# Kernel tuning notes

Measured on AMD Instinct MI355X. Metric: run time of the kernel, lower is better.

## Reference

```python
import jax, jax.numpy as jnp
import numpy as np

GROUP_SIZES = [5, 5, 5, 5, 5, 5, 4]  # 7 concept groups, sum = 34
LN_EPS = 1e-5


def setup_inputs() -> dict:
    key = jax.random.key(0)
    ks = jax.random.split(key, 12)
    B, N, D, K, P, C, NC, H = 256, 196, 768, 7, 512, 34, 7, 3072
    img_feat_map = jax.random.normal(ks[0], (B, N, D), dtype=jnp.float32)
    # torch: Embedding weight uniform in [-1/K, 1/K]
    vq_codebook = (jax.random.uniform(ks[1], (K, D), dtype=jnp.float32) * 2.0 - 1.0) / K
    agg_codebook = jax.random.normal(ks[2], (K, D), dtype=jnp.float32)
    W1 = jax.random.normal(ks[3], (D, H), dtype=jnp.float32) * 0.02
    b1 = jnp.zeros((H,), dtype=jnp.float32)
    W2 = jax.random.normal(ks[4], (H, D), dtype=jnp.float32) * 0.02
    b2 = jnp.zeros((D,), dtype=jnp.float32)
    ln_gamma = jnp.ones((D,), dtype=jnp.float32)
    ln_beta = jnp.zeros((D,), dtype=jnp.float32)
    W_proj = jax.random.normal(ks[5], (D, P), dtype=jnp.float32) * 0.02
    concept_emb = jax.random.normal(ks[6], (C, P), dtype=jnp.float32)
    concept_emb = concept_emb / jnp.linalg.norm(concept_emb, axis=-1, keepdims=True)
    cls_W = jax.random.normal(ks[7], (C, NC), dtype=jnp.float32) * 0.02
    cls_b = jnp.zeros((NC,), dtype=jnp.float32)
    logit_scale = jnp.float32(100.0)  # detached CLIP logit scale
    return {
        "img_feat_map": img_feat_map, "vq_codebook": vq_codebook,
        "agg_codebook": agg_codebook, "W1": W1, "b1": b1, "W2": W2, "b2": b2,
        "ln_gamma": ln_gamma, "ln_beta": ln_beta, "W_proj": W_proj,
        "concept_emb": concept_emb, "cls_W": cls_W, "cls_b": cls_b,
        "logit_scale": logit_scale,
    }


def _pairwise_sq_dists(x, cb):
    # x: [B, N, D], cb: [K, D] -> [B, N, K]
    x_sq = jnp.sum(x * x, axis=-1, keepdims=True)           # [B, N, 1]
    cb_sq = jnp.sum(cb * cb, axis=-1)                        # [K]
    dot = jnp.einsum("bnd,kd->bnk", x, cb)                  # [B, N, K]
    return x_sq + cb_sq - 2.0 * dot


def _avg_effective_rank(x, threshold=0.99):
    # x: [B, N, D]; per-sample SVD, rank = #{cumsum(S)/sum(S) <= thr}
    S = jnp.linalg.svd(jax.lax.stop_gradient(x), compute_uv=False)  # [B, min(N,D)]
    energy = jnp.cumsum(S, axis=-1) / jnp.sum(S, axis=-1, keepdims=True)
    ranks = jnp.sum(energy <= threshold, axis=-1)
    return jnp.mean(ranks.astype(jnp.float32))


def reference(img_feat_map, vq_codebook, agg_codebook, W1, b1, W2, b2,
              ln_gamma, ln_beta, W_proj, concept_emb, cls_W, cls_b, logit_scale):
    x = img_feat_map  # [B, N, D]

    avg_rank = _avg_effective_rank(x)

    # --- VectorQuantizeAggregator: soft assignment to 7 codes ---
    d_agg = _pairwise_sq_dists(x, agg_codebook)              # [B, N, K]
    soft = jax.nn.softmax(-d_agg, axis=-1)                   # [B, N, K]
    agg = jnp.einsum("bnk,bnd->bkd", soft, x)               # [B, K, D]

    # --- VectorQuantizer: hard argmin + gather (one-hot @ codebook) ---
    d_vq = _pairwise_sq_dists(x, vq_codebook)                # [B, N, K]
    idx = jnp.argmin(d_vq, axis=-1)                          # [B, N] int
    quantized = vq_codebook[idx]                             # [B, N, D] gather == onehot @ cb
    sg = jax.lax.stop_gradient
    codebook_loss = jnp.mean((quantized - sg(x)) ** 2)
    commitment_loss = jnp.mean((sg(quantized) - x) ** 2)
    vq_loss = codebook_loss + 1.0 * commitment_loss

    # --- bridge: FFN -> LayerNorm -> proj -> L2 normalize ---
    h = jax.nn.gelu(agg @ W1 + b1, approximate=False) @ W2 + b2  # [B, K, D]
    mu = jnp.mean(h, axis=-1, keepdims=True)
    var = jnp.mean((h - mu) ** 2, axis=-1, keepdims=True)
    hn = (h - mu) * jax.lax.rsqrt(var + LN_EPS) * ln_gamma + ln_beta
    tok = hn @ W_proj                                        # [B, K, 512]
    tok = tok / jnp.linalg.norm(tok, axis=-1, keepdims=True)

    # --- per-group concept logits: token g vs its concept slice ---
    logits_list = []
    start = 0
    for g, sz in enumerate(GROUP_SIZES):
        ce = concept_emb[start:start + sz]                   # [sz, 512]
        logits_list.append(logit_scale * (tok[:, g, :] @ ce.T))  # [B, sz]
        start += sz
    image_logits = jnp.concatenate(logits_list, axis=-1)     # [B, 34]

    cls_logits = image_logits @ cls_W + cls_b                # [B, 7]
    return (cls_logits, image_logits, vq_loss, avg_rank)
```

## Files before the change

kernel.cpp:

```cpp
#include <hip/hip_runtime.h>
#include <hip/hip_bf16.h>
#include <math.h>

using hbf = __hip_bfloat16;
typedef __bf16 bf16x8 __attribute__((ext_vector_type(8)));
typedef float f32x4 __attribute__((ext_vector_type(4)));

__device__ inline float wred(float v){
#pragma unroll
  for (int o = 32; o > 0; o >>= 1) v += __shfl_xor(v, o);
  return v;
}
__device__ inline float r16(float v){
  v += __shfl_xor(v, 1); v += __shfl_xor(v, 2);
  v += __shfl_xor(v, 4); v += __shfl_xor(v, 8);
  return v;
}
__device__ inline float fast_rcp(float x){
  float r; asm("v_rcp_f32 %0, %1" : "=v"(r) : "v"(x)); return r;
}
__device__ inline float d4(const float4& a, const float4& b){
  return a.x*b.x + a.y*b.y + a.z*b.z + a.w*b.w;
}

__global__ void k_init(float* scal){
  if (threadIdx.x < 2) scal[threadIdx.x] = 0.f;
}

__global__ __launch_bounds__(512) void k_dist(const float* __restrict__ x,
    const float* __restrict__ vqcb, const float* __restrict__ agcb,
    hbf* __restrict__ aggbf, float* __restrict__ scal){
  __shared__ float cA[5376];
  __shared__ float cV[5376];
  __shared__ float sqA[7], sqV[7];
  const int tid = threadIdx.x, lane = tid & 63, wave = tid >> 6;
  const int b = blockIdx.x;
  for (int i = tid; i < 5376; i += 512){ cA[i] = agcb[i]; cV[i] = vqcb[i]; }
  __syncthreads();
  {
    int grp = tid >> 4, l16 = tid & 15;
    if (grp < 14){
      const float* s = (grp < 7) ? &cA[grp*768] : &cV[(grp-7)*768];
      float acc = 0.f;
      for (int j = l16; j < 768; j += 16) acc += s[j]*s[j];
      acc = r16(acc);
      if (l16 == 0){ if (grp < 7) sqA[grp] = acc; else sqV[grp-7] = acc; }
    }
  }
  __syncthreads();
  float sqAr[7], sqVr[7];
#pragma unroll
  for (int k = 0; k < 7; ++k){ sqAr[k] = sqA[k]; sqVr[k] = sqV[k]; }

  float4 aR[7][3];
#pragma unroll
  for (int k = 0; k < 7; ++k)
#pragma unroll
    for (int c = 0; c < 3; ++c) aR[k][c] = make_float4(0.f,0.f,0.f,0.f);
  float loss = 0.f;

  const float* xb = x + (size_t)b*196*768;
  float4 cx0, cx1, cx2, nx0, nx1, nx2;
  { const float* p = xb + (size_t)wave*768 + (lane<<2);
    cx0 = *(const float4*)(p); cx1 = *(const float4*)(p+256); cx2 = *(const float4*)(p+512); }
  for (int it = 0; it < 25; ++it){
    const int n = it*8 + wave;
    const int nn = n + 8;
    if (nn < 196){
      const float* p = xb + (size_t)nn*768 + (lane<<2);
      nx0 = *(const float4*)(p); nx1 = *(const float4*)(p+256); nx2 = *(const float4*)(p+512);
    }
    if (n < 196){
      float xsq = d4(cx0,cx0)+d4(cx1,cx1)+d4(cx2,cx2);
      float dA[7], dV[7];
#pragma unroll
      for (int k = 0; k < 7; ++k){
        const float4* pa = (const float4*)&cA[k*768];
        const float4* pv = (const float4*)&cV[k*768];
        float4 a0 = pa[lane], a1 = pa[64+lane], a2 = pa[128+lane];
        float4 q0 = pv[lane], q1 = pv[64+lane], q2 = pv[128+lane];
        dA[k] = d4(cx0,a0)+d4(cx1,a1)+d4(cx2,a2);
        dV[k] = d4(cx0,q0)+d4(cx1,q1)+d4(cx2,q2);
      }
      xsq = wred(xsq);
#pragma unroll
      for (int k = 0; k < 7; ++k){ dA[k] = wred(dA[k]); dV[k] = wred(dV[k]); }
      float lg[7], mx = -1e30f;
#pragma unroll
      for (int k = 0; k < 7; ++k){ lg[k] = 2.f*dA[k] - sqAr[k]; mx = fmaxf(mx, lg[k]); }
      float pr[7], ssum = 0.f;
#pragma unroll
      for (int k = 0; k < 7; ++k){ pr[k] = expf(lg[k]-mx); ssum += pr[k]; }
      const float inv = 1.f/ssum;
      float mn = 1e30f;
#pragma unroll
      for (int k = 0; k < 7; ++k) mn = fminf(mn, sqVr[k] - 2.f*dV[k]);
      loss += xsq + mn;
#pragma unroll
      for (int k = 0; k < 7; ++k){
        const float w = pr[k]*inv;
        aR[k][0].x += w*cx0.x; aR[k][0].y += w*cx0.y; aR[k][0].z += w*cx0.z; aR[k][0].w += w*cx0.w;
        aR[k][1].x += w*cx1.x; aR[k][1].y += w*cx1.y; aR[k][1].z += w*cx1.z; aR[k][1].w += w*cx1.w;
        aR[k][2].x += w*cx2.x; aR[k][2].y += w*cx2.y; aR[k][2].z += w*cx2.z; aR[k][2].w += w*cx2.w;
      }
    }
    cx0 = nx0; cx1 = nx1; cx2 = nx2;
  }
  __syncthreads();
  for (int i = tid; i < 5376; i += 512) cA[i] = 0.f;
  __syncthreads();
  for (int w = 0; w < 8; ++w){
    if (wave == w){
#pragma unroll
      for (int k = 0; k < 7; ++k)
#pragma unroll
        for (int c = 0; c < 3; ++c){
          float* p = &cA[k*768 + c*256 + (lane<<2)];
          p[0] += aR[k][c].x; p[1] += aR[k][c].y; p[2] += aR[k][c].z; p[3] += aR[k][c].w;
        }
    }
    __syncthreads();
  }
  for (int i = tid; i < 5376; i += 512) aggbf[(size_t)b*5376 + i] = __float2bfloat16(cA[i]);
  if (lane == 0) atomicAdd(&scal[0], loss);
}

__global__ __launch_bounds__(512) void k_gram(const float* __restrict__ x, float* __restrict__ G){
  __shared__ hbf Xs[208*104];
  const int tid = threadIdx.x, lane = tid & 63, wave = tid >> 6;
  const int b = blockIdx.x;
  const int l15 = lane & 15;
  const int fr0 = wave, fr1 = wave + 8;
  const bool f1 = (fr1 < 13);
  f32x4 acc0[13] = {};
  f32x4 acc1[13] = {};
  const float* xb = x + (size_t)b*196*768;
  for (int kc = 0; kc < 8; ++kc){
    __syncthreads();
    for (int u = tid; u < 4992; u += 512){
      const int r = u / 24, c4 = u - r*24;
      ushort4 val;
      if (r < 196){
        float4 f = *(const float4*)(xb + (size_t)r*768 + kc*96 + c4*4);
        hbf t0 = __float2bfloat16(f.x), t1 = __float2bfloat16(f.y);
        hbf t2 = __float2bfloat16(f.z), t3 = __float2bfloat16(f.w);
        val.x = *(const unsigned short*)&t0; val.y = *(const unsigned short*)&t1;
        val.z = *(const unsigned short*)&t2; val.w = *(const unsigned short*)&t3;
      } else { val.x = 0; val.y = 0; val.z = 0; val.w = 0; }
      *(ushort4*)&Xs[r*104 + c4*4] = val;
    }
    __syncthreads();
#pragma unroll
    for (int kk = 0; kk < 3; ++kk){
      const int ko = kk*32 + (lane>>4)*8;
      bf16x8 a0 = *(const bf16x8*)&Xs[(fr0*16 + l15)*104 + ko];
      bf16x8 a1 = f1 ? *(const bf16x8*)&Xs[(fr1*16 + l15)*104 + ko] : a0;
#pragma unroll
      for (int fc = 0; fc < 13; ++fc){
        bf16x8 bb = *(const bf16x8*)&Xs[(fc*16 + l15)*104 + ko];
        acc0[fc] = __builtin_amdgcn_mfma_f32_16x16x32_bf16(a0, bb, acc0[fc], 0, 0, 0);
        if (f1) acc1[fc] = __builtin_amdgcn_mfma_f32_16x16x32_bf16(a1, bb, acc1[fc], 0, 0, 0);
      }
    }
  }
  const size_t gb = (size_t)b*38416;
  const int cr = (lane>>4)*4;
#pragma unroll
  for (int fc = 0; fc < 13; ++fc){
    const int gc = fc*16 + l15;
    if (gc < 196){
#pragma unroll
      for (int r = 0; r < 4; ++r){
        const int gr = fr0*16 + cr + r;
        if (gr < 196) G[gb + (size_t)gr*196 + gc] = acc0[fc][r];
      }
      if (f1){
#pragma unroll
        for (int r = 0; r < 4; ++r){
          const int gr = fr1*16 + cr + r;
          if (gr < 196) G[gb + (size_t)gr*196 + gc] = acc1[fc][r];
        }
      }
    }
  }
}

__global__ __launch_bounds__(1024) void k_eigen(const float* __restrict__ G, float* __restrict__ scal){
  extern __shared__ float S[];
  float* A   = S;
  float* ww  = S + 38496;
  float* dd  = S + 38752;
  float* ee  = S + 38952;
  float* e2  = S + 39152;
  float* red2= S + 39352;
  const int n = 196;
  const int tid = threadIdx.x, lane = tid & 63, wave = tid >> 6;
  const int grp = lane >> 4, c16 = lane & 15;
  const int b = blockIdx.x;
  {
    const float4* Gv = (const float4*)(G + (size_t)b*38416);
    float4* Av = (float4*)A;
    for (int u = tid; u < 9604; u += 1024) Av[u] = Gv[u];
    if (tid < 80) S[38416 + tid] = 0.f;
  }
  __syncthreads();
  for (int k = 0; k <= n-3; ++k){
    const int base = k + 1, m = n - 1 - k;
    const float* rowk = &A[(size_t)k*196];
    const float x0 = rowk[base];
    float4 v4[4];
    float sig = 0.f;
#pragma unroll
    for (int p = 0; p < 4; ++p){
      const int col = (p << 6) + (c16 << 2);
      float4 xv = *(const float4*)(rowk + col);
      xv.x = (col+0 > base && col+0 < n) ? xv.x : 0.f;
      xv.y = (col+1 > base && col+1 < n) ? xv.y : 0.f;
      xv.z = (col+2 > base && col+2 < n) ? xv.z : 0.f;
      xv.w = (col+3 > base && col+3 < n) ? xv.w : 0.f;
      v4[p] = xv;
      sig += xv.x*xv.x + xv.y*xv.y + xv.z*xv.z + xv.w*xv.w;
    }
    sig = r16(sig);
    float tau = 0.f, v0 = 0.f, alpha = x0;
    if (sig > 1e-20f){
      const float mu = sqrtf(x0*x0 + sig);
      alpha = (x0 > 0.f) ? -mu : mu;
      v0 = x0 - alpha;
      tau = 2.f/(sig + v0*v0);
    }
    if (tid == 0) ee[k] = alpha;
#pragma unroll
    for (int p = 0; p < 4; ++p){
      const int col = (p << 6) + (c16 << 2);
      v4[p].x = (col+0 == base) ? v0 : v4[p].x;
      v4[p].y = (col+1 == base) ? v0 : v4[p].y;
      v4[p].z = (col+2 == base) ? v0 : v4[p].z;
      v4[p].w = (col+3 == base) ? v0 : v4[p].w;
    }
    const int p0 = base >> 6;
    const int nsw = (m + 63) >> 6;
    if (tau != 0.f){
      float cpart = 0.f;
      for (int t = 0; t < nsw; ++t){
        const int i = (t << 6) + (wave << 2) + grp;
        float acc = 0.f;
        if (i < m){
          const float* Ar = &A[(size_t)(base+i)*196];
#pragma unroll
          for (int p = 0; p < 4; ++p){
            if (p >= p0){
              const int col = (p << 6) + (c16 << 2);
              const float4 a4 = *(const float4*)(Ar + col);
              acc += a4.x*v4[p].x + a4.y*v4[p].y + a4.z*v4[p].z + a4.w*v4[p].w;
            }
          }
        }
        acc = r16(acc);
        if (i < m && c16 == 0){
          const float wr = tau*acc;
          ww[base+i] = wr;
          cpart += ((i == 0) ? v0 : rowk[base+i])*wr;
        }
      }
      cpart += __shfl_xor(cpart, 16);
      cpart += __shfl_xor(cpart, 32);
      if (lane == 0) red2[wave] = cpart;
    }
    __syncthreads();
    if (tau != 0.f){
      const float4* r2 = (const float4*)red2;
      const float4 q0 = r2[0], q1 = r2[1], q2 = r2[2], q3 = r2[3];
      const float vtw = (q0.x+q0.y+q0.z+q0.w) + (q1.x+q1.y+q1.z+q1.w)
                      + (q2.x+q2.y+q2.z+q2.w) + (q3.x+q3.y+q3.z+q3.w);
      const float c2 = 0.5f*tau*vtw;
      float4 w4[4];
#pragma unroll
      for (int p = 0; p < 4; ++p){
        const int col = (p << 6) + (c16 << 2);
        const float4 t4 = *(const float4*)(ww + col);
        w4[p].x = (col+0 >= base && col+0 < n) ? (t4.x - c2*v4[p].x) : 0.f;
        w4[p].y = (col+1 >= base && col+1 < n) ? (t4.y - c2*v4[p].y) : 0.f;
        w4[p].z = (col+2 >= base && col+2 < n) ? (t4.z - c2*v4[p].z) : 0.f;
        w4[p].w = (col+3 >= base && col+3 < n) ? (t4.w - c2*v4[p].w) : 0.f;
      }
      for (int t = 0; t < nsw; ++t){
        const int i = (t << 6) + (wave << 2) + grp;
        if (i < m){
          const float vi = (i == 0) ? v0 : rowk[base+i];
          const float wi = ww[base+i] - c2*vi;
          float* Ar = &A[(size_t)(base+i)*196];
#pragma unroll
          for (int p = 0; p < 4; ++p){
            if (p >= p0){
              const int col = (p << 6) + (c16 << 2);
              float4 a4 = *(const float4*)(Ar + col);
              a4.x -= vi*w4[p].x + wi*v4[p].x;
              a4.y -= vi*w4[p].y + wi*v4[p].y;
              a4.z -= vi*w4[p].z + wi*v4[p].z;
              a4.w -= vi*w4[p].w + wi*v4[p].w;
              *(float4*)(Ar + col) = a4;
            }
          }
        }
      }
    }
    __syncthreads();
  }
  if (tid < n) dd[tid] = A[(size_t)tid*196 + tid];
  if (tid == 0) ee[n-2] = A[(size_t)(n-1)*196 + (n-2)];
  __syncthreads();
  if (tid < n-1) e2[tid] = ee[tid]*ee[tid];
  __syncthreads();
  float lo = 1e30f, hi = -1e30f;
  if (tid < n){
    const float rr = ((tid > 0) ? fabsf(ee[tid-1]) : 0.f) + ((tid < n-1) ? fabsf(ee[tid]) : 0.f);
    lo = dd[tid] - rr; hi = dd[tid] + rr;
  }
  {
    float l2 = lo, h2 = hi;
#pragma unroll
    for (int o = 32; o > 0; o >>= 1){
      l2 = fminf(l2, __shfl_xor(l2, o));
      h2 = fmaxf(h2, __shfl_xor(h2, o));
    }
    if (lane == 0){ ww[wave] = l2; red2[wave] = h2; }
  }
  __syncthreads();
  float glo = ww[0], ghi = red2[0];
#pragma unroll
  for (int w2 = 1; w2 < 16; ++w2){ glo = fminf(glo, ww[w2]); ghi = fmaxf(ghi, red2[w2]); }
  __syncthreads();
  float sv = 0.f;
  if (tid < n){
    float lob = glo, hib = ghi;
    for (int it2 = 0; it2 < 26; ++it2){
      const float mid = 0.5f*(lob + hib);
      float q = dd[0] - mid;
      int cnt = (q < 0.f) ? 1 : 0;
      for (int i = 1; i < n; ++i){
        const float r = fast_rcp(q);
        q = (dd[i] - mid) - e2[i-1]*r;
        q = (fabsf(q) < 1e-6f) ? -1e-6f : q;
        cnt += (q < 0.f) ? 1 : 0;
      }
      if (cnt <= tid) lob = mid; else hib = mid;
    }
    sv = sqrtf(fmaxf(0.5f*(lob + hib), 0.f));
  }
  __syncthreads();
  if (tid < n) ww[tid] = sv;
  __syncthreads();
  if (tid == 0){
    float tot = 0.f;
    for (int i = 0; i < n; ++i) tot += ww[i];
    const float thr = 0.99f*tot;
    float cs = 0.f; int rank = 0;
    for (int i = n-1; i >= 0; --i){ cs += ww[i]; rank += (cs <= thr) ? 1 : 0; }
    atomicAdd(&scal[1], (float)rank);
  }
}

__global__ __launch_bounds__(256) void k_tr(const float* __restrict__ in, hbf* __restrict__ outp,
                                            int Rr, int Cc){
  __shared__ float t[32][33];
  const int tid = threadIdx.x;
  const int lc = tid & 31, lr = tid >> 5;
  const int c0 = blockIdx.x*32, r0 = blockIdx.y*32;
#pragma unroll
  for (int i = 0; i < 4; ++i)
    t[lr + i*8][lc] = in[(size_t)(r0 + lr + i*8)*Cc + c0 + lc];
  __syncthreads();
#pragma unroll
  for (int i = 0; i < 4; ++i)
    outp[(size_t)(c0 + lr + i*8)*Rr + r0 + lc] = __float2bfloat16(t[lc][lr + i*8]);
}

template<int EPI>
__global__ __launch_bounds__(256) void k_gemm(const hbf* __restrict__ Aa, const hbf* __restrict__ Bb,
    const float* __restrict__ bias, void* __restrict__ outp, int Mi, int Ni, int Ki){
  __shared__ hbf As[64*72];
  __shared__ hbf Bs[64*72];
  const int tid = threadIdx.x, lane = tid & 63, wave = tid >> 6;
  const int row0 = blockIdx.y*64, col0 = blockIdx.x*64;
  const int m0 = (wave >> 1)*32, n0 = (wave & 1)*32;
  const int l15 = lane & 15, lk = (lane >> 4)*8;
  const int sr = tid >> 3, sc = (tid & 7)*8;
  f32x4 acc00 = {}, acc01 = {}, acc10 = {}, acc11 = {};
  for (int kt = 0; kt < Ki; kt += 64){
    __syncthreads();
    *(uint4*)&As[sr*72 + sc]        = *(const uint4*)&Aa[(size_t)(row0+sr)*Ki + kt + sc];
    *(uint4*)&As[(sr+32)*72 + sc]   = *(const uint4*)&Aa[(size_t)(row0+sr+32)*Ki + kt + sc];
    *(uint4*)&Bs[sr*72 + sc]        = *(const uint4*)&Bb[(size_t)(col0+sr)*Ki + kt + sc];
    *(uint4*)&Bs[(sr+32)*72 + sc]   = *(const uint4*)&Bb[(size_t)(col0+sr+32)*Ki + kt + sc];
    __syncthreads();
#pragma unroll
    for (int kk = 0; kk < 2; ++kk){
      const int ko = kk*32 + lk;
      bf16x8 a0 = *(const bf16x8*)&As[(m0 + l15)*72 + ko];
      bf16x8 a1 = *(const bf16x8*)&As[(m0 + 16 + l15)*72 + ko];
      bf16x8 b0 = *(const bf16x8*)&Bs[(n0 + l15)*72 + ko];
      bf16x8 b1 = *(const bf16x8*)&Bs[(n0 + 16 + l15)*72 + ko];
      acc00 = __builtin_amdgcn_mfma_f32_16x16x32_bf16(a0, b0, acc00, 0, 0, 0);
      acc01 = __builtin_amdgcn_mfma_f32_16x16x32_bf16(a0, b1, acc01, 0, 0, 0);
      acc10 = __builtin_amdgcn_mfma_f32_16x16x32_bf16(a1, b0, acc10, 0, 0, 0);
      acc11 = __builtin_amdgcn_mfma_f32_16x16x32_bf16(a1, b1, acc11, 0, 0, 0);
    }
  }
  const int cr = (lane >> 4)*4;
#pragma unroll
  for (int i = 0; i < 2; ++i){
#pragma unroll
    for (int j = 0; j < 2; ++j){
      f32x4 av = (i == 0) ? ((j == 0) ? acc00 : acc01) : ((j == 0) ? acc10 : acc11);
      const int gcol = col0 + n0 + j*16 + l15;
#pragma unroll
      for (int r = 0; r < 4; ++r){
        const int grow = row0 + m0 + i*16 + cr + r;
        float v = av[r];
        if (EPI == 1){
          v += bias[gcol];
          v = 0.5f*v*(1.f + erff(v*0.70710678118654752f));
          ((hbf*)outp)[(size_t)grow*Ni + gcol] = __float2bfloat16(v);
        } else if (EPI == 2){
          v += bias[gcol];
          ((float*)outp)[(size_t)grow*Ni + gcol] = v;
        } else {
          ((float*)outp)[(size_t)grow*Ni + gcol] = v;
        }
      }
    }
  }
}

__global__ __launch_bounds__(256) void k_ln(const float* __restrict__ h, const float* __restrict__ gam,
    const float* __restrict__ bet, hbf* __restrict__ hn){
  const int tid = threadIdx.x, lane = tid & 63, wave = tid >> 6;
  const int row = blockIdx.x*4 + wave;
  const float* hr = h + (size_t)row*768;
  const int off = lane*4;
  float4 v0 = *(const float4*)(hr + off);
  float4 v1 = *(const float4*)(hr + 256 + off);
  float4 v2 = *(const float4*)(hr + 512 + off);
  float s = v0.x+v0.y+v0.z+v0.w + v1.x+v1.y+v1.z+v1.w + v2.x+v2.y+v2.z+v2.w;
  s = wred(s);
  const float mu = s*(1.f/768.f);
  float q = 0.f;
  q += (v0.x-mu)*(v0.x-mu); q += (v0.y-mu)*(v0.y-mu); q += (v0.z-mu)*(v0.z-mu); q += (v0.w-mu)*(v0.w-mu);
  q += (v1.x-mu)*(v1.x-mu); q += (v1.y-mu)*(v1.y-mu); q += (v1.z-mu)*(v1.z-mu); q += (v1.w-mu)*(v1.w-mu);
  q += (v2.x-mu)*(v2.x-mu); q += (v2.y-mu)*(v2.y-mu); q += (v2.z-mu)*(v2.z-mu); q += (v2.w-mu)*(v2.w-mu);
  q = wred(q);
  const float rs = 1.f/sqrtf(q*(1.f/768.f) + 1e-5f);
  float4 g0 = *(const float4*)(gam + off), g1 = *(const float4*)(gam + 256 + off), g2 = *(const float4*)(gam + 512 + off);
  float4 t0 = *(const float4*)(bet + off), t1 = *(const float4*)(bet + 256 + off), t2 = *(const float4*)(bet + 512 + off);
  hbf* o = hn + (size_t)row*768;
  o[off+0] = __float2bfloat16((v0.x-mu)*rs*g0.x + t0.x);
  o[off+1] = __float2bfloat16((v0.y-mu)*rs*g0.y + t0.y);
  o[off+2] = __float2bfloat16((v0.z-mu)*rs*g0.z + t0.z);
  o[off+3] = __float2bfloat16((v0.w-mu)*rs*g0.w + t0.w);
  o[256+off+0] = __float2bfloat16((v1.x-mu)*rs*g1.x + t1.x);
  o[256+off+1] = __float2bfloat16((v1.y-mu)*rs*g1.y + t1.y);
  o[256+off+2] = __float2bfloat16((v1.z-mu)*rs*g1.z + t1.z);
  o[256+off+3] = __float2bfloat16((v1.w-mu)*rs*g1.w + t1.w);
  o[512+off+0] = __float2bfloat16((v2.x-mu)*rs*g2.x + t2.x);
  o[512+off+1] = __float2bfloat16((v2.y-mu)*rs*g2.y + t2.y);
  o[512+off+2] = __float2bfloat16((v2.z-mu)*rs*g2.z + t2.z);
  o[512+off+3] = __float2bfloat16((v2.w-mu)*rs*g2.w + t2.w);
}

__global__ __launch_bounds__(256) void k_head(const float* __restrict__ tok, const float* __restrict__ ce,
    const float* __restrict__ clsW, const float* __restrict__ clsb, const float* __restrict__ lgs,
    float* __restrict__ out){
  __shared__ float tkn[7*512];
  __shared__ float il[40];
  const int tid = threadIdx.x, lane = tid & 63, wave = tid >> 6;
  const int b = blockIdx.x;
  const float ls = lgs[0];
  for (int g = wave; g < 7; g += 4){
    const float* tr = tok + (size_t)(b*7 + g)*512;
    float4 u0 = *(const float4*)(tr + (lane<<3));
    float4 u1 = *(const float4*)(tr + (lane<<3) + 4);
    float s = d4(u0,u0) + d4(u1,u1);
    s = wred(s);
    const float inv = 1.f/sqrtf(s);
    float* dst = &tkn[g*512 + (lane<<3)];
    dst[0] = u0.x*inv; dst[1] = u0.y*inv; dst[2] = u0.z*inv; dst[3] = u0.w*inv;
    dst[4] = u1.x*inv; dst[5] = u1.y*inv; dst[6] = u1.z*inv; dst[7] = u1.w*inv;
  }
  __syncthreads();
  for (int c = wave; c < 34; c += 4){
    const int g = (c < 30) ? (c/5) : 6;
    const float* tp = &tkn[g*512 + (lane<<3)];
    const float* cp = ce + (size_t)c*512 + (lane<<3);
    float s = tp[0]*cp[0] + tp[1]*cp[1] + tp[2]*cp[2] + tp[3]*cp[3]
            + tp[4]*cp[4] + tp[5]*cp[5] + tp[6]*cp[6] + tp[7]*cp[7];
    s = wred(s);
    if (lane == 0){
      const float v = ls*s;
      il[c] = v;
      out[1792 + b*34 + c] = v;
    }
  }
  __syncthreads();
  if (tid < 7){
    float s = clsb[tid];
    for (int c = 0; c < 34; ++c) s += il[c]*clsW[c*7 + tid];
    out[b*7 + tid] = s;
  }
}

__global__ void k_fin(const float* __restrict__ scal, float* __restrict__ out){
  if (threadIdx.x == 0){
    out[10496] = 2.f*scal[0]/(float)(256*196*768);
    out[10497] = scal[1]*(1.f/256.f);
  }
}

extern "C" void kernel_launch(void* const* d_in, const int* in_sizes, int n_in,
                              void* d_out, int out_size, void* d_ws, size_t ws_size,
                              hipStream_t stream) {
  (void)in_sizes; (void)n_in; (void)out_size; (void)ws_size;
  const float* x    = (const float*)d_in[0];
  const float* vqcb = (const float*)d_in[1];
  const float* agcb = (const float*)d_in[2];
  const float* W1   = (const float*)d_in[3];
  const float* b1   = (const float*)d_in[4];
  const float* W2   = (const float*)d_in[5];
  const float* b2   = (const float*)d_in[6];
  const float* gam  = (const float*)d_in[7];
  const float* bet  = (const float*)d_in[8];
  const float* Wp   = (const float*)d_in[9];
  const float* ce   = (const float*)d_in[10];
  const float* clsW = (const float*)d_in[11];
  const float* clsb = (const float*)d_in[12];
  const float* lgs  = (const float*)d_in[13];
  float* out = (float*)d_out;
  char* w = (char*)d_ws;

  float* scal  = (float*)w;
  float* G     = (float*)(w + 256);
  hbf*   aggbf = (hbf*)(w + 39338240ULL);
  hbf*   W1t   = (hbf*)(w + 42090752ULL);
  hbf*   W2t   = (hbf*)(w + 46809344ULL);
  hbf*   Wpt   = (hbf*)(w + 51527936ULL);
  hbf*   h1    = (hbf*)(w + 256);
  float* hbuf  = (float*)(w + 256 + 16777216ULL);
  hbf*   hn    = (hbf*)(w + 256 + 25165824ULL);
  float* tok   = (float*)(w + 256 + 29360128ULL);

  k_init<<<dim3(1), dim3(64), 0, stream>>>(scal);
  k_dist<<<dim3(256), dim3(512), 0, stream>>>(x, vqcb, agcb, aggbf, scal);
  k_gram<<<dim3(256), dim3(512), 0, stream>>>(x, G);
  const int EIG_SMEM = 39368*4;
  hipFuncSetAttribute((const void*)k_eigen, hipFuncAttributeMaxDynamicSharedMemorySize, EIG_SMEM);
  k_eigen<<<dim3(256), dim3(1024), EIG_SMEM, stream>>>(G, scal);
  k_tr<<<dim3(96,24), dim3(256), 0, stream>>>(W1, W1t, 768, 3072);
  k_tr<<<dim3(24,96), dim3(256), 0, stream>>>(W2, W2t, 3072, 768);
  k_tr<<<dim3(16,24), dim3(256), 0, stream>>>(Wp, Wpt, 768, 512);
  k_gemm<1><<<dim3(48,28), dim3(256), 0, stream>>>(aggbf, W1t, b1, (void*)h1, 1792, 3072, 768);
  k_gemm<2><<<dim3(12,28), dim3(256), 0, stream>>>(h1, W2t, b2, (void*)hbuf, 1792, 768, 3072);
  k_ln<<<dim3(448), dim3(256), 0, stream>>>(hbuf, gam, bet, hn);
  k_gemm<3><<<dim3(8,28), dim3(256), 0, stream>>>(hn, Wpt, nullptr, (void*)tok, 1792, 512, 768);
  k_head<<<dim3(256), dim3(256), 0, stream>>>(tok, ce, clsW, clsb, lgs, out);
  k_fin<<<dim3(1), dim3(64), 0, stream>>>(scal, out);
}
```

Before: 1.114 ms.

## Specialize Householder tridiagonalization: DPP reductions, unrolled tiles, single-wave tail

The Householder tridiagonalization loop in the eigen kernel is rewritten with the four column tiles fully unrolled, and the row dot-products and outer values are kept in registers between the matvec and rank-2 update phases instead of being recomputed from shared memory. The 16-lane reductions now use DPP row shifts instead of shuffles. For the last steps (k>130), where the trailing submatrix has at most 64 rows, only wave 0 does the work with wave-local fences, removing the block-wide barriers in that phase. This relies on exact assumptions about n=196 and the column layout, and the serial single-wave tail leaves the other waves idle.

```diff
diff --git a/kernel.cpp b/kernel.cpp
--- a/kernel.cpp
+++ b/kernel.cpp
@@ -6,14 +6,22 @@
 typedef __bf16 bf16x8 __attribute__((ext_vector_type(8)));
 typedef float f32x4 __attribute__((ext_vector_type(4)));
 
+__device__ inline float r16d(float v){
+  int x;
+  x = __builtin_bit_cast(int, v);
+  v += __builtin_bit_cast(float, __builtin_amdgcn_mov_dpp(x, 0x121, 0xf, 0xf, true));
+  x = __builtin_bit_cast(int, v);
+  v += __builtin_bit_cast(float, __builtin_amdgcn_mov_dpp(x, 0x122, 0xf, 0xf, true));
+  x = __builtin_bit_cast(int, v);
+  v += __builtin_bit_cast(float, __builtin_amdgcn_mov_dpp(x, 0x124, 0xf, 0xf, true));
+  x = __builtin_bit_cast(int, v);
+  v += __builtin_bit_cast(float, __builtin_amdgcn_mov_dpp(x, 0x128, 0xf, 0xf, true));
+  return v;
+}
 __device__ inline float wred(float v){
-#pragma unroll
-  for (int o = 32; o > 0; o >>= 1) v += __shfl_xor(v, o);
-  return v;
-}
-__device__ inline float r16(float v){
-  v += __shfl_xor(v, 1); v += __shfl_xor(v, 2);
-  v += __shfl_xor(v, 4); v += __shfl_xor(v, 8);
+  v = r16d(v);
+  v += __shfl_xor(v, 16);
+  v += __shfl_xor(v, 32);
   return v;
 }
 __device__ inline float fast_rcp(float x){
@@ -43,7 +51,7 @@
       const float* s = (grp < 7) ? &cA[grp*768] : &cV[(grp-7)*768];
       float acc = 0.f;
       for (int j = l16; j < 768; j += 16) acc += s[j]*s[j];
-      acc = r16(acc);
+      acc = r16d(acc);
       if (l16 == 0){ if (grp < 7) sqA[grp] = acc; else sqV[grp-7] = acc; }
     }
   }
@@ -185,6 +193,20 @@
   }
 }
 
+#define FOLD4(vv4) { vv4.x = (oc==0)? v0 : vv4.x; vv4.y = (oc==1)? v0 : vv4.y; \
+                     vv4.z = (oc==2)? v0 : vv4.z; vv4.w = (oc==3)? v0 : vv4.w; }
+#define VHOIST(colc, out) { \
+  const int col_ = (colc) + jc4; \
+  const float4 xv_ = *(const float4*)(rowk + col_); \
+  float4 vp_; \
+  if (col_ > base){ vp_ = xv_; } \
+  else if (col_ + 3 <= base){ vp_ = make_float4(0.f,0.f,0.f,0.f); } \
+  else { vp_.x = 0.f; \
+         vp_.y = (col_+1 > base) ? xv_.y : 0.f; \
+         vp_.z = (col_+2 > base) ? xv_.z : 0.f; \
+         vp_.w = xv_.w; } \
+  out = vp_; sig += vp_.x*vp_.x + vp_.y*vp_.y + vp_.z*vp_.z + vp_.w*vp_.w; }
+
 __global__ __launch_bounds__(1024) void k_eigen(const float* __restrict__ G, float* __restrict__ scal){
   extern __shared__ float S[];
   float* A   = S;
@@ -196,32 +218,34 @@
   const int n = 196;
   const int tid = threadIdx.x, lane = tid & 63, wave = tid >> 6;
   const int grp = lane >> 4, c16 = lane & 15;
+  const int jc4 = c16 << 2;
+  const int rbase = (wave << 2) + grp;
   const int b = blockIdx.x;
   {
     const float4* Gv = (const float4*)(G + (size_t)b*38416);
     float4* Av = (float4*)A;
     for (int u = tid; u < 9604; u += 1024) Av[u] = Gv[u];
     if (tid < 80) S[38416 + tid] = 0.f;
-  }
-  __syncthreads();
-  for (int k = 0; k <= n-3; ++k){
+    if (tid < 256) ww[tid] = 0.f;
+  }
+  __syncthreads();
+  for (int k = 0; k <= 130; ++k){
     const int base = k + 1, m = n - 1 - k;
     const float* rowk = &A[(size_t)k*196];
     const float x0 = rowk[base];
-    float4 v4[4];
+    if (tid == 0) ww[k] = 0.f;
+    float4 v4_0, v4_1, v4_2, v4_3;
     float sig = 0.f;
-#pragma unroll
-    for (int p = 0; p < 4; ++p){
-      const int col = (p << 6) + (c16 << 2);
-      float4 xv = *(const float4*)(rowk + col);
-      xv.x = (col+0 > base && col+0 < n) ? xv.x : 0.f;
-      xv.y = (col+1 > base && col+1 < n) ? xv.y : 0.f;
-      xv.z = (col+2 > base && col+2 < n) ? xv.z : 0.f;
-      xv.w = (col+3 > base && col+3 < n) ? xv.w : 0.f;
-      v4[p] = xv;
-      sig += xv.x*xv.x + xv.y*xv.y + xv.z*xv.z + xv.w*xv.w;
-    }
-    sig = r16(sig);
+    VHOIST(0,   v4_0)
+    VHOIST(64,  v4_1)
+    VHOIST(128, v4_2)
+    {
+      const int col_ = 192 + jc4;
+      const float4 xv_ = *(const float4*)(rowk + col_);
+      if (c16 == 0){ v4_3 = xv_; sig += xv_.x*xv_.x + xv_.y*xv_.y + xv_.z*xv_.z + xv_.w*xv_.w; }
+      else v4_3 = make_float4(0.f,0.f,0.f,0.f);
+    }
+    sig = r16d(sig);
     float tau = 0.f, v0 = 0.f, alpha = x0;
     if (sig > 1e-20f){
       const float mu = sqrtf(x0*x0 + sig);
@@ -230,39 +254,35 @@
       tau = 2.f/(sig + v0*v0);
     }
     if (tid == 0) ee[k] = alpha;
-#pragma unroll
-    for (int p = 0; p < 4; ++p){
-      const int col = (p << 6) + (c16 << 2);
-      v4[p].x = (col+0 == base) ? v0 : v4[p].x;
-      v4[p].y = (col+1 == base) ? v0 : v4[p].y;
-      v4[p].z = (col+2 == base) ? v0 : v4[p].z;
-      v4[p].w = (col+3 == base) ? v0 : v4[p].w;
+    if (c16 == ((base >> 2) & 15)){
+      const int oc = base & 3;
+      const int op = base >> 6;
+      if (op == 0){ FOLD4(v4_0) } else if (op == 1){ FOLD4(v4_1) } else { FOLD4(v4_2) }
     }
     const int p0 = base >> 6;
-    const int nsw = (m + 63) >> 6;
+    float vr_0=0.f, vr_1=0.f, vr_2=0.f, vr_3=0.f;
+    float wr_0=0.f, wr_1=0.f, wr_2=0.f, wr_3=0.f;
     if (tau != 0.f){
       float cpart = 0.f;
-      for (int t = 0; t < nsw; ++t){
-        const int i = (t << 6) + (wave << 2) + grp;
-        float acc = 0.f;
-        if (i < m){
-          const float* Ar = &A[(size_t)(base+i)*196];
-#pragma unroll
-          for (int p = 0; p < 4; ++p){
-            if (p >= p0){
-              const int col = (p << 6) + (c16 << 2);
-              const float4 a4 = *(const float4*)(Ar + col);
-              acc += a4.x*v4[p].x + a4.y*v4[p].y + a4.z*v4[p].z + a4.w*v4[p].w;
-            }
-          }
-        }
-        acc = r16(acc);
-        if (i < m && c16 == 0){
-          const float wr = tau*acc;
-          ww[base+i] = wr;
-          cpart += ((i == 0) ? v0 : rowk[base+i])*wr;
-        }
-      }
+#define MV_T(T, VRV, WRV) { \
+      const int i_ = ((T)<<6) + rbase; \
+      if (i_ < m){ \
+        const float* Ar = &A[(size_t)(base+i_)*196]; \
+        float acc = 0.f; \
+        if (0 >= p0){ const float4 a = *(const float4*)(Ar + jc4);       acc += d4(a, v4_0); } \
+        if (1 >= p0){ const float4 a = *(const float4*)(Ar + 64 + jc4);  acc += d4(a, v4_1); } \
+        if (2 >= p0){ const float4 a = *(const float4*)(Ar + 128 + jc4); acc += d4(a, v4_2); } \
+        { const float4 a = *(const float4*)(Ar + 192 + jc4);             acc += d4(a, v4_3); } \
+        acc = r16d(acc); \
+        WRV = tau*acc; \
+        VRV = (i_ == 0) ? v0 : rowk[base+i_]; \
+        cpart += VRV*WRV; \
+        if (c16 == 0) ww[base+i_] = WRV; } }
+      MV_T(0, vr_0, wr_0)
+      MV_T(1, vr_1, wr_1)
+      MV_T(2, vr_2, wr_2)
+      MV_T(3, vr_3, wr_3)
+#undef MV_T
       cpart += __shfl_xor(cpart, 16);
       cpart += __shfl_xor(cpart, 32);
       if (lane == 0) red2[wave] = cpart;
@@ -274,39 +294,133 @@
       const float vtw = (q0.x+q0.y+q0.z+q0.w) + (q1.x+q1.y+q1.z+q1.w)
                       + (q2.x+q2.y+q2.z+q2.w) + (q3.x+q3.y+q3.z+q3.w);
       const float c2 = 0.5f*tau*vtw;
-      float4 w4[4];
-#pragma unroll
-      for (int p = 0; p < 4; ++p){
-        const int col = (p << 6) + (c16 << 2);
-        const float4 t4 = *(const float4*)(ww + col);
-        w4[p].x = (col+0 >= base && col+0 < n) ? (t4.x - c2*v4[p].x) : 0.f;
-        w4[p].y = (col+1 >= base && col+1 < n) ? (t4.y - c2*v4[p].y) : 0.f;
-        w4[p].z = (col+2 >= base && col+2 < n) ? (t4.z - c2*v4[p].z) : 0.f;
-        w4[p].w = (col+3 >= base && col+3 < n) ? (t4.w - c2*v4[p].w) : 0.f;
-      }
-      for (int t = 0; t < nsw; ++t){
-        const int i = (t << 6) + (wave << 2) + grp;
-        if (i < m){
-          const float vi = (i == 0) ? v0 : rowk[base+i];
-          const float wi = ww[base+i] - c2*vi;
-          float* Ar = &A[(size_t)(base+i)*196];
-#pragma unroll
-          for (int p = 0; p < 4; ++p){
-            if (p >= p0){
-              const int col = (p << 6) + (c16 << 2);
-              float4 a4 = *(const float4*)(Ar + col);
-              a4.x -= vi*w4[p].x + wi*v4[p].x;
-              a4.y -= vi*w4[p].y + wi*v4[p].y;
-              a4.z -= vi*w4[p].z + wi*v4[p].z;
-              a4.w -= vi*w4[p].w + wi*v4[p].w;
-              *(float4*)(Ar + col) = a4;
+      float4 w4_0, w4_1, w4_2, w4_3;
+      { const float4 t4 = *(const float4*)(ww + jc4);
+        w4_0.x = t4.x - c2*v4_0.x; w4_0.y = t4.y - c2*v4_0.y; w4_0.z = t4.z - c2*v4_0.z; w4_0.w = t4.w - c2*v4_0.w; }
+      { const float4 t4 = *(const float4*)(ww + 64 + jc4);
+        w4_1.x = t4.x - c2*v4_1.x; w4_1.y = t4.y - c2*v4_1.y; w4_1.z = t4.z - c2*v4_1.z; w4_1.w = t4.w - c2*v4_1.w; }
+      { const float4 t4 = *(const float4*)(ww + 128 + jc4);
+        w4_2.x = t4.x - c2*v4_2.x; w4_2.y = t4.y - c2*v4_2.y; w4_2.z = t4.z - c2*v4_2.z; w4_2.w = t4.w - c2*v4_2.w; }
+      { const float4 t4 = *(const float4*)(ww + 192 + jc4);
+        w4_3.x = t4.x - c2*v4_3.x; w4_3.y = t4.y - c2*v4_3.y; w4_3.z = t4.z - c2*v4_3.z; w4_3.w = t4.w - c2*v4_3.w; }
+#define UP_T(T, VRV, WRV) { \
+      const int i_ = ((T)<<6) + rbase; \
+      if (i_ < m){ \
+        const float vi = VRV; \
+        const float wi = WRV - c2*vi; \
+        float* Ar = &A[(size_t)(base+i_)*196]; \
+        if (0 >= p0){ float4 a = *(const float4*)(Ar + jc4); \
+          a.x -= vi*w4_0.x + wi*v4_0.x; a.y -= vi*w4_0.y + wi*v4_0.y; \
+          a.z -= vi*w4_0.z + wi*v4_0.z; a.w -= vi*w4_0.w + wi*v4_0.w; \
+          *(float4*)(Ar + jc4) = a; } \
+        if (1 >= p0){ float4 a = *(const float4*)(Ar + 64 + jc4); \
+          a.x -= vi*w4_1.x + wi*v4_1.x; a.y -= vi*w4_1.y + wi*v4_1.y; \
+          a.z -= vi*w4_1.z + wi*v4_1.z; a.w -= vi*w4_1.w + wi*v4_1.w; \
+          *(float4*)(Ar + 64 + jc4) = a; } \
+        if (2 >= p0){ float4 a = *(const float4*)(Ar + 128 + jc4); \
+          a.x -= vi*w4_2.x + wi*v4_2.x; a.y -= vi*w4_2.y + wi*v4_2.y; \
+          a.z -= vi*w4_2.z + wi*v4_2.z; a.w -= vi*w4_2.w + wi*v4_2.w; \
+          *(float4*)(Ar + 128 + jc4) = a; } \
+        if (c16 == 0){ float4 a = *(const float4*)(Ar + 192); \
+          a.x -= vi*w4_3.x + wi*v4_3.x; a.y -= vi*w4_3.y + wi*v4_3.y; \
+          a.z -= vi*w4_3.z + wi*v4_3.z; a.w -= vi*w4_3.w + wi*v4_3.w; \
+          *(float4*)(Ar + 192) = a; } } }
+      UP_T(0, vr_0, wr_0)
+      UP_T(1, vr_1, wr_1)
+      UP_T(2, vr_2, wr_2)
+      UP_T(3, vr_3, wr_3)
+#undef UP_T
+    }
+    __syncthreads();
+  }
+  if (wave == 0){
+    float vrT[16], wrT[16];
+    for (int k = 131; k <= n-3; ++k){
+      const int base = k + 1, m = n - 1 - k;
+      const float* rowk = &A[(size_t)k*196];
+      const float x0 = rowk[base];
+      if (lane == 0) ww[k] = 0.f;
+      float4 v4_2, v4_3;
+      float sig = 0.f;
+      VHOIST(128, v4_2)
+      {
+        const int col_ = 192 + jc4;
+        float4 vp_ = make_float4(0.f,0.f,0.f,0.f);
+        if (c16 == 0){
+          const float4 xv_ = *(const float4*)(rowk + col_);
+          if (col_ > base){ vp_ = xv_; }
+          else { vp_.x = 0.f;
+                 vp_.y = (col_+1 > base) ? xv_.y : 0.f;
+                 vp_.z = (col_+2 > base) ? xv_.z : 0.f;
+                 vp_.w = xv_.w; }
+        }
+        v4_3 = vp_; sig += vp_.x*vp_.x + vp_.y*vp_.y + vp_.z*vp_.z + vp_.w*vp_.w;
+      }
+      sig = r16d(sig);
+      float tau = 0.f, v0 = 0.f, alpha = x0;
+      if (sig > 1e-20f){
+        const float mu = sqrtf(x0*x0 + sig);
+        alpha = (x0 > 0.f) ? -mu : mu;
+        v0 = x0 - alpha;
+        tau = 2.f/(sig + v0*v0);
+      }
+      if (lane == 0) ee[k] = alpha;
+      if (c16 == ((base >> 2) & 15)){
+        const int oc = base & 3;
+        if ((base >> 6) == 2){ FOLD4(v4_2) } else { FOLD4(v4_3) }
+      }
+      if (tau != 0.f){
+        float cpart = 0.f;
+#pragma unroll
+        for (int t = 0; t < 16; ++t){
+          const int i_ = (t << 2) + grp;
+          float vrv = 0.f, wrv = 0.f;
+          if (i_ < m){
+            const float* Ar = &A[(size_t)(base+i_)*196];
+            const float4 a2 = *(const float4*)(Ar + 128 + jc4);
+            const float4 a3 = *(const float4*)(Ar + 192 + jc4);
+            float acc = d4(a2, v4_2) + d4(a3, v4_3);
+            acc = r16d(acc);
+            wrv = tau*acc;
+            vrv = (i_ == 0) ? v0 : rowk[base+i_];
+            cpart += vrv*wrv;
+            if (c16 == 0) ww[base+i_] = wrv;
+          }
+          vrT[t] = vrv; wrT[t] = wrv;
+        }
+        cpart += __shfl_xor(cpart, 16);
+        cpart += __shfl_xor(cpart, 32);
+        const float c2 = 0.5f*tau*cpart;
+        __threadfence_block();
+        float4 w4_2, w4_3;
+        { const float4 t4 = *(const float4*)(ww + 128 + jc4);
+          w4_2.x = t4.x - c2*v4_2.x; w4_2.y = t4.y - c2*v4_2.y; w4_2.z = t4.z - c2*v4_2.z; w4_2.w = t4.w - c2*v4_2.w; }
+        { const float4 t4 = *(const float4*)(ww + 192 + jc4);
+          w4_3.x = t4.x - c2*v4_3.x; w4_3.y = t4.y - c2*v4_3.y; w4_3.z = t4.z - c2*v4_3.z; w4_3.w = t4.w - c2*v4_3.w; }
+#pragma unroll
+        for (int t = 0; t < 16; ++t){
+          const int i_ = (t << 2) + grp;
+          if (i_ < m){
+            const float vi = vrT[t];
+            const float wi = wrT[t] - c2*vi;
+            float* Ar = &A[(size_t)(base+i_)*196];
+            float4 a = *(const float4*)(Ar + 128 + jc4);
+            a.x -= vi*w4_2.x + wi*v4_2.x; a.y -= vi*w4_2.y + wi*v4_2.y;
+            a.z -= vi*w4_2.z + wi*v4_2.z; a.w -= vi*w4_2.w + wi*v4_2.w;
+            *(float4*)(Ar + 128 + jc4) = a;
+            if (c16 == 0){
+              float4 a3 = *(const float4*)(Ar + 192);
+              a3.x -= vi*w4_3.x + wi*v4_3.x; a3.y -= vi*w4_3.y + wi*v4_3.y;
+              a3.z -= vi*w4_3.z + wi*v4_3.z; a3.w -= vi*w4_3.w + wi*v4_3.w;
+              *(float4*)(Ar + 192) = a3;
             }
           }
         }
-      }
-    }
-    __syncthreads();
-  }
+        __threadfence_block();
+      }
+    }
+  }
+  __syncthreads();
   if (tid < n) dd[tid] = A[(size_t)tid*196 + tid];
   if (tid == 0) ee[n-2] = A[(size_t)(n-1)*196 + (n-2)];
   __syncthreads();
```

Result: faster. 1.049 ms (-5.9%).
